# Kernel optimization log

Measured on AMD Instinct MI355X. Metric: run time of the kernel, lower is better.

## Reference

```python
import jax, jax.numpy as jnp
import numpy as np


def _kan_layer(comb, W1, b1, W2, b2, Wc, bc):
    # comb: [B, D]; W1,b1,W2: [D, K]; b2: [D]; Wc: [D, H]; bc: [H]
    # per-feature MLP: Linear(1,K) -> ReLU -> Linear(K,1), batched over D
    h = jax.nn.relu(comb[:, :, None] * W1[None, :, :] + b1[None, :, :])  # [B, D, K]
    u = jnp.einsum('bdk,dk->bd', h, W2) + b2[None, :]                    # [B, D]
    return u @ Wc + bc[None, :]                                          # [B, H]


def setup_inputs() -> dict:
    key = jax.random.key(0)
    ks = jax.random.split(key, 9)
    B, I, H, K = 2048, 256, 512, 32
    D = I + H
    s = 0.05
    return {
        'x': jax.random.normal(ks[0], (B, I), dtype=jnp.float32),
        'h_prev': jax.random.normal(ks[1], (B, H), dtype=jnp.float32),
        'c_prev': jax.random.normal(ks[2], (B, H), dtype=jnp.float32),
        'W1': jax.random.normal(ks[3], (4, D, K), dtype=jnp.float32) * s,
        'b1': jax.random.normal(ks[4], (4, D, K), dtype=jnp.float32) * s,
        'W2': jax.random.normal(ks[5], (4, D, K), dtype=jnp.float32) * s,
        'b2': jax.random.normal(ks[6], (4, D), dtype=jnp.float32) * s,
        'Wc': jax.random.normal(ks[7], (4, D, H), dtype=jnp.float32) * s,
        'bc': jax.random.normal(ks[8], (4, H), dtype=jnp.float32) * s,
    }


def reference(x, h_prev, c_prev, W1, b1, W2, b2, Wc, bc):
    comb = jnp.concatenate([x, h_prev], axis=1)  # [B, D]
    # gate order: 0=forget, 1=input, 2=output, 3=cell
    gates = [_kan_layer(comb, W1[g], b1[g], W2[g], b2[g], Wc[g], bc[g])
             for g in range(4)]
    f_t = jax.nn.sigmoid(gates[0])
    i_t = jax.nn.sigmoid(gates[1])
    o_t = jax.nn.sigmoid(gates[2])
    c_tilde = jnp.tanh(gates[3])
    c_t = f_t * c_prev + i_t * c_tilde
    h_t = o_t * jnp.tanh(c_t)
    return (h_t, c_t)
```

## Files before the change

### kernel.cpp

```cpp
#include <hip/hip_runtime.h>

#define B_  2048
#define I_  256
#define H_  512
#define D_  768
#define K_  32

typedef unsigned short ushort_t;
typedef unsigned int uint_t;
typedef __attribute__((ext_vector_type(8))) __bf16 bf16x8;
typedef __attribute__((ext_vector_type(4))) float f32x4;

__device__ __forceinline__ ushort_t f2bf(float f) {
  uint_t u = __float_as_uint(f);
  u += 0x7fffu + ((u >> 16) & 1u);
  return (ushort_t)(u >> 16);
}
__device__ __forceinline__ float fast_sigmoid(float x) {
  return 1.f / (1.f + __expf(-x));
}
__device__ __forceinline__ float fast_tanh(float x) {
  float t = __expf(2.f * fabsf(x));
  float r = 1.f - 2.f / (t + 1.f);
  return copysignf(r, x);
}
__device__ __forceinline__ void gload16(const void* g, void* l) {
  __builtin_amdgcn_global_load_lds(
      (const __attribute__((address_space(1))) void*)g,
      (__attribute__((address_space(3))) void*)l, 16, 0, 0);
}

__global__ __launch_bounds__(256) void kan_prep(
    const float* __restrict__ x, const float* __restrict__ hp,
    const float* __restrict__ W1, const float* __restrict__ b1,
    const float* __restrict__ W2, const float* __restrict__ b2,
    const float* __restrict__ Wc,
    ushort_t* __restrict__ wcT, ushort_t* __restrict__ uT) {
  __shared__ float ttile[32][33];
  int bid = blockIdx.x;
  if (bid < 1536) {
    int tx = threadIdx.x & 31, ty = threadIdx.x >> 5;
    int g = bid / 384;
    int rem = bid % 384;
    int d0 = (rem / 16) * 32;
    int h0 = (rem % 16) * 32;
#pragma unroll
    for (int i = 0; i < 4; ++i) {
      int r = ty + i * 8;
      ttile[r][tx] = Wc[((size_t)g * D_ + d0 + r) * H_ + h0 + tx];
    }
    __syncthreads();
#pragma unroll
    for (int i = 0; i < 4; ++i) {
      int r = ty + i * 8;
      wcT[((size_t)g * H_ + h0 + r) * D_ + d0 + tx] = f2bf(ttile[tx][r]);
    }
  } else {
    int p = bid - 1536;
    int combo = p >> 6;
    int bc = p & 63;
    int g = combo & 3;
    int dc = combo >> 2;
    int t = threadIdx.x;
    int d = dc * 256 + t;

    f32x4 w1v[8], bbv[8], w2v[8];
    const float* W1p = W1 + ((size_t)g * D_ + d) * K_;
    const float* b1p = b1 + ((size_t)g * D_ + d) * K_;
    const float* W2p = W2 + ((size_t)g * D_ + d) * K_;
#pragma unroll
    for (int q = 0; q < 8; ++q) {
      w1v[q] = *(const f32x4*)(W1p + q * 4);
      bbv[q] = *(const f32x4*)(b1p + q * 4);
      w2v[q] = *(const f32x4*)(W2p + q * 4);
    }
    float bias = b2[(size_t)g * D_ + d];

    const float* src = (dc == 0) ? (x + t) : (hp + ((dc == 1) ? t : t + 256));
    int stride = (dc == 0) ? I_ : H_;
    int b0 = bc * 32;

#pragma unroll
    for (int bb8 = 0; bb8 < 32; bb8 += 8) {
      float cv[8], acc[8];
#pragma unroll
      for (int j = 0; j < 8; ++j) {
        cv[j] = src[(size_t)(b0 + bb8 + j) * stride];
        acc[j] = bias;
      }
#pragma unroll
      for (int q = 0; q < 8; ++q)
#pragma unroll
        for (int e = 0; e < 4; ++e) {
          float w1 = w1v[q][e], bbk = bbv[q][e], w2 = w2v[q][e];
#pragma unroll
          for (int j = 0; j < 8; ++j) {
            float h = fmaxf(fmaf(cv[j], w1, bbk), 0.f);
            acc[j] = fmaf(h, w2, acc[j]);
          }
        }
#pragma unroll
      for (int j = 0; j < 8; ++j)
        uT[((size_t)g * B_ + b0 + bb8 + j) * D_ + d] = f2bf(acc[j]);
    }
  }
}

#define TBM 64
#define THN 64
#define BK2 32
#define NT2 (D_ / BK2)
#define AREG 16384
#define BUF2 32768
#define NBUF2 4

__global__ __launch_bounds__(1024, 4) void kan_phase2(
    const ushort_t* __restrict__ uT, const ushort_t* __restrict__ wcT,
    const float* __restrict__ bc, const float* __restrict__ cprev,
    float* __restrict__ out) {
  __shared__ __align__(16) char smem[NBUF2 * BUF2];
  const int b0 = blockIdx.x * TBM;
  const int h0 = blockIdx.y * THN;
  const int t = threadIdx.x;
  const int w = t >> 6;
  const int l = t & 63;
  const int g = w >> 2, mh = w & 3;
  const int frow = l & 15, c0 = l >> 4;

  const int srow = t >> 2, sc = t & 3;
  const int sg = srow >> 6, sr = srow & 63;
  const int scg = sc ^ ((sr ^ (sr >> 2)) & 3);
  const ushort_t* asrc = uT + ((size_t)sg * B_ + b0 + sr) * D_ + scg * 8;
  const ushort_t* bsrc = wcT + ((size_t)sg * H_ + h0 + sr) * D_ + scg * 8;
  const int aLds = t * 16;
  const int bLds = AREG + t * 16;

  const int key = (frow ^ (frow >> 2)) & 3;
  const int cx = ((c0 ^ key) << 4);
  const int aoff = ((g * 64 + mh * 16 + frow) << 6) + cx;
  int boff[4];
#pragma unroll
  for (int n = 0; n < 4; ++n)
    boff[n] = AREG + ((g * 64 + n * 16 + frow) << 6) + cx;

  f32x4 acc[4];
#pragma unroll
  for (int n = 0; n < 4; ++n) {
    float bv = bc[(size_t)g * H_ + h0 + n * 16 + frow];
    acc[n] = (f32x4){bv, bv, bv, bv};
  }

  auto stage = [&](int bufoff, int ke) {
    gload16(asrc + ke, smem + bufoff + aLds);
    gload16(bsrc + ke, smem + bufoff + bLds);
  };
  auto compute = [&](const char* bb) {
    bf16x8 af = *(const bf16x8*)(bb + aoff);
    bf16x8 bf[4];
#pragma unroll
    for (int n = 0; n < 4; ++n) bf[n] = *(const bf16x8*)(bb + boff[n]);
    __builtin_amdgcn_s_setprio(1);
#pragma unroll
    for (int n = 0; n < 4; ++n)
      acc[n] = __builtin_amdgcn_mfma_f32_16x16x32_bf16(af, bf[n], acc[n], 0, 0, 0);
    __builtin_amdgcn_s_setprio(0);
  };

  stage(0 * BUF2, 0 * BK2);
  stage(1 * BUF2, 1 * BK2);
  stage(2 * BUF2, 2 * BK2);
  int s = 0;
  for (; s < NT2 - 3; ++s) {
    asm volatile("s_waitcnt vmcnt(4)" ::: "memory");
    __builtin_amdgcn_s_barrier();
    stage(((s + 3) & 3) * BUF2, (s + 3) * BK2);
    compute(smem + (s & 3) * BUF2);
  }
  asm volatile("s_waitcnt vmcnt(4)" ::: "memory");
  __builtin_amdgcn_s_barrier();
  compute(smem + (s & 3) * BUF2);
  ++s;
  asm volatile("s_waitcnt vmcnt(2)" ::: "memory");
  __builtin_amdgcn_s_barrier();
  compute(smem + (s & 3) * BUF2);
  ++s;
  asm volatile("s_waitcnt vmcnt(0)" ::: "memory");
  __builtin_amdgcn_s_barrier();
  compute(smem + (s & 3) * BUF2);
  __syncthreads();

  float* gf = (float*)smem;
#pragma unroll
  for (int n = 0; n < 4; ++n)
#pragma unroll
    for (int e = 0; e < 4; ++e) {
      int row = mh * 16 + c0 * 4 + e;
      int col = n * 16 + frow;
      gf[((size_t)g * 64 + row) * 68 + col] = acc[n][e];
    }
  __syncthreads();

  {
    int row = t >> 4;
    int ch = t & 15;
    int b = b0 + row;
    int hc = h0 + ch * 4;
    f32x4 g0 = *(const f32x4*)&gf[((size_t)0 * 64 + row) * 68 + ch * 4];
    f32x4 g1 = *(const f32x4*)&gf[((size_t)1 * 64 + row) * 68 + ch * 4];
    f32x4 g2 = *(const f32x4*)&gf[((size_t)2 * 64 + row) * 68 + ch * 4];
    f32x4 g3 = *(const f32x4*)&gf[((size_t)3 * 64 + row) * 68 + ch * 4];
    f32x4 cp = *(const f32x4*)&cprev[(size_t)b * H_ + hc];
    f32x4 hv, cv;
#pragma unroll
    for (int e = 0; e < 4; ++e) {
      float ft = fast_sigmoid(g0[e]);
      float it = fast_sigmoid(g1[e]);
      float ot = fast_sigmoid(g2[e]);
      float tc = fast_tanh(g3[e]);
      float cn = ft * cp[e] + it * tc;
      cv[e] = cn;
      hv[e] = ot * fast_tanh(cn);
    }
    *(f32x4*)&out[(size_t)b * H_ + hc] = hv;
    *(f32x4*)&out[(size_t)B_ * H_ + (size_t)b * H_ + hc] = cv;
  }
}

extern "C" void kernel_launch(void* const* d_in, const int* in_sizes, int n_in,
                              void* d_out, int out_size, void* d_ws, size_t ws_size,
                              hipStream_t stream) {
  const float* x  = (const float*)d_in[0];
  const float* hp = (const float*)d_in[1];
  const float* cp = (const float*)d_in[2];
  const float* W1 = (const float*)d_in[3];
  const float* b1 = (const float*)d_in[4];
  const float* W2 = (const float*)d_in[5];
  const float* b2 = (const float*)d_in[6];
  const float* Wc = (const float*)d_in[7];
  const float* bc = (const float*)d_in[8];
  float* out = (float*)d_out;

  ushort_t* wcT = (ushort_t*)d_ws;
  ushort_t* uT  = wcT + (size_t)4 * H_ * D_;

  kan_prep<<<2304, 256, 0, stream>>>(x, hp, W1, b1, W2, b2, Wc, wcT, uT);
  kan_phase2<<<dim3(B_ / TBM, H_ / THN), 1024, 0, stream>>>(uT, wcT, bc, cp, out);
}
```

Baseline: 47.17 us.

## Split prep into weight transpose and MLP kernels with K-major weight layout

The combined prep kernel is split in two. A transpose kernel lays W1/b1/W2 out K-major (alongside the Wc bf16 transpose) so that MLP threads read per-k weights with coalesced loads instead of each thread holding 96 weight registers. The MLP kernel now handles 32 batch rows per thread, streaming weights in chunks of 4 k values. This adds a kernel launch and a round trip through workspace for the transposed weights, and the 32-row batch loop raises register pressure.

```diff
diff --git a/kernel.cpp b/kernel.cpp
--- a/kernel.cpp
+++ b/kernel.cpp
@@ -30,80 +30,100 @@
       (__attribute__((address_space(3))) void*)l, 16, 0, 0);
 }
 
-__global__ __launch_bounds__(256) void kan_prep(
-    const float* __restrict__ x, const float* __restrict__ hp,
+__global__ __launch_bounds__(256) void transpose_all(
     const float* __restrict__ W1, const float* __restrict__ b1,
-    const float* __restrict__ W2, const float* __restrict__ b2,
-    const float* __restrict__ Wc,
-    ushort_t* __restrict__ wcT, ushort_t* __restrict__ uT) {
-  __shared__ float ttile[32][33];
+    const float* __restrict__ W2, const float* __restrict__ Wc,
+    float* __restrict__ w1t, float* __restrict__ b1t, float* __restrict__ w2t,
+    ushort_t* __restrict__ wcT) {
+  __shared__ float t[32][33];
+  int tx = threadIdx.x & 31, ty = threadIdx.x >> 5;
   int bid = blockIdx.x;
-  if (bid < 1536) {
-    int tx = threadIdx.x & 31, ty = threadIdx.x >> 5;
-    int g = bid / 384;
-    int rem = bid % 384;
+  if (bid < 288) {
+    int z = bid / 96;
+    int g = (bid / 24) % 4;
+    int d0 = (bid % 24) * 32;
+    const float* src = (z == 0) ? W1 : (z == 1) ? b1 : W2;
+    float* dst       = (z == 0) ? w1t : (z == 1) ? b1t : w2t;
+#pragma unroll
+    for (int i = 0; i < 4; ++i) {
+      int r = ty + i * 8;
+      t[r][tx] = src[((size_t)g * D_ + d0 + r) * K_ + tx];
+    }
+    __syncthreads();
+#pragma unroll
+    for (int i = 0; i < 4; ++i) {
+      int r = ty + i * 8;
+      dst[((size_t)g * K_ + r) * D_ + d0 + tx] = t[tx][r];
+    }
+  } else {
+    int r2 = bid - 288;
+    int g = r2 / 384;
+    int rem = r2 % 384;
     int d0 = (rem / 16) * 32;
     int h0 = (rem % 16) * 32;
 #pragma unroll
     for (int i = 0; i < 4; ++i) {
       int r = ty + i * 8;
-      ttile[r][tx] = Wc[((size_t)g * D_ + d0 + r) * H_ + h0 + tx];
+      t[r][tx] = Wc[((size_t)g * D_ + d0 + r) * H_ + h0 + tx];
     }
     __syncthreads();
 #pragma unroll
     for (int i = 0; i < 4; ++i) {
       int r = ty + i * 8;
-      wcT[((size_t)g * H_ + h0 + r) * D_ + d0 + tx] = f2bf(ttile[tx][r]);
-    }
-  } else {
-    int p = bid - 1536;
-    int combo = p >> 6;
-    int bc = p & 63;
-    int g = combo & 3;
-    int dc = combo >> 2;
-    int t = threadIdx.x;
-    int d = dc * 256 + t;
-
-    f32x4 w1v[8], bbv[8], w2v[8];
-    const float* W1p = W1 + ((size_t)g * D_ + d) * K_;
-    const float* b1p = b1 + ((size_t)g * D_ + d) * K_;
-    const float* W2p = W2 + ((size_t)g * D_ + d) * K_;
-#pragma unroll
-    for (int q = 0; q < 8; ++q) {
-      w1v[q] = *(const f32x4*)(W1p + q * 4);
-      bbv[q] = *(const f32x4*)(b1p + q * 4);
-      w2v[q] = *(const f32x4*)(W2p + q * 4);
-    }
-    float bias = b2[(size_t)g * D_ + d];
-
-    const float* src = (dc == 0) ? (x + t) : (hp + ((dc == 1) ? t : t + 256));
-    int stride = (dc == 0) ? I_ : H_;
-    int b0 = bc * 32;
-
-#pragma unroll
-    for (int bb8 = 0; bb8 < 32; bb8 += 8) {
-      float cv[8], acc[8];
-#pragma unroll
-      for (int j = 0; j < 8; ++j) {
-        cv[j] = src[(size_t)(b0 + bb8 + j) * stride];
-        acc[j] = bias;
+      wcT[((size_t)g * H_ + h0 + r) * D_ + d0 + tx] = f2bf(t[tx][r]);
+    }
+  }
+}
+
+__global__ __launch_bounds__(256) void kan_mlp(
+    const float* __restrict__ x, const float* __restrict__ hp,
+    const float* __restrict__ w1t, const float* __restrict__ b1t,
+    const float* __restrict__ w2t, const float* __restrict__ b2,
+    ushort_t* __restrict__ uT) {
+  int bi = blockIdx.x;
+  int combo = bi >> 6;
+  int bc = bi & 63;
+  int g = combo & 3;
+  int dc = combo >> 2;
+  int t = threadIdx.x;
+  int d = dc * 256 + t;
+
+  const float* src = (dc == 0) ? (x + t) : (hp + ((dc == 1) ? t : t + 256));
+  int stride = (dc == 0) ? I_ : H_;
+  int b0 = bc * 32;
+
+  float cv[32], acc[32];
+  float bias = b2[(size_t)g * D_ + d];
+#pragma unroll
+  for (int j = 0; j < 32; ++j) {
+    cv[j] = src[(size_t)(b0 + j) * stride];
+    acc[j] = bias;
+  }
+
+  const float* w1p = w1t + (size_t)g * K_ * D_ + d;
+  const float* b1p = b1t + (size_t)g * K_ * D_ + d;
+  const float* w2p = w2t + (size_t)g * K_ * D_ + d;
+
+  for (int kc = 0; kc < K_; kc += 4) {
+    float w1c[4], b1c[4], w2c[4];
+#pragma unroll
+    for (int e = 0; e < 4; ++e) {
+      w1c[e] = w1p[(size_t)(kc + e) * D_];
+      b1c[e] = b1p[(size_t)(kc + e) * D_];
+      w2c[e] = w2p[(size_t)(kc + e) * D_];
+    }
+#pragma unroll
+    for (int e = 0; e < 4; ++e)
+#pragma unroll
+      for (int j = 0; j < 32; ++j) {
+        float h = fmaxf(fmaf(cv[j], w1c[e], b1c[e]), 0.f);
+        acc[j] = fmaf(h, w2c[e], acc[j]);
       }
-#pragma unroll
-      for (int q = 0; q < 8; ++q)
-#pragma unroll
-        for (int e = 0; e < 4; ++e) {
-          float w1 = w1v[q][e], bbk = bbv[q][e], w2 = w2v[q][e];
-#pragma unroll
-          for (int j = 0; j < 8; ++j) {
-            float h = fmaxf(fmaf(cv[j], w1, bbk), 0.f);
-            acc[j] = fmaf(h, w2, acc[j]);
-          }
-        }
-#pragma unroll
-      for (int j = 0; j < 8; ++j)
-        uT[((size_t)g * B_ + b0 + bb8 + j) * D_ + d] = f2bf(acc[j]);
-    }
-  }
+  }
+
+  ushort_t* up = uT + (size_t)g * B_ * D_ + (size_t)b0 * D_ + d;
+#pragma unroll
+  for (int j = 0; j < 32; ++j) up[(size_t)j * D_] = f2bf(acc[j]);
 }
 
 #define TBM 64
@@ -240,9 +260,13 @@
   const float* bc = (const float*)d_in[8];
   float* out = (float*)d_out;
 
-  ushort_t* wcT = (ushort_t*)d_ws;
+  float* w1t = (float*)d_ws;
+  float* b1t = w1t + 98304;
+  float* w2t = b1t + 98304;
+  ushort_t* wcT = (ushort_t*)(w2t + 98304);
   ushort_t* uT  = wcT + (size_t)4 * H_ * D_;
 
-  kan_prep<<<2304, 256, 0, stream>>>(x, hp, W1, b1, W2, b2, Wc, wcT, uT);
+  transpose_all<<<1824, 256, 0, stream>>>(W1, b1, W2, Wc, w1t, b1t, w2t, wcT);
+  kan_mlp<<<768, 256, 0, stream>>>(x, hp, w1t, b1t, w2t, b2, uT);
   kan_phase2<<<dim3(B_ / TBM, H_ / THN), 1024, 0, stream>>>(uT, wcT, bc, cp, out);
 }
```

Result: slower. 50.40 us (+6.9%).
